# Kernel tuning notes

Hardware: AMD Instinct MI355X
Metric: run time of the kernel (lower is better)

The kernel has to match this reference:

```python
import jax, jax.numpy as jnp
import numpy as np

B, C, M, N = 8, 64, 256, 256
THRESHOLD = 0.8
EPS = 1e-5
PAD = 3  # kernel_size=7


def conv2d(x, w, b=None):
    # x: (B,Cin,H,W), w: (Cout,Cin,7,7), stride 1, 'same' padding 3
    y = jax.lax.conv_general_dilated(
        x, w, window_strides=(1, 1), padding=[(PAD, PAD), (PAD, PAD)],
        dimension_numbers=('NCHW', 'OIHW', 'NCHW'))
    if b is not None:
        y = y + b[None, :, None, None]
    return y


def region_norm(region, mask):
    # region: (B,C,M,N) zeroed outside region; mask: (B,C,M,N) binary
    s = jnp.sum(region, axis=(0, 2, 3))            # (C,)
    Sr = jnp.sum(mask, axis=(0, 2, 3))             # (C,)
    Sr = jnp.where(Sr == 0, 1.0, Sr)
    mu = (s / Sr)[None, :, None, None]
    t = region + (1.0 - mask) * mu                 # fill surroundings with region mean
    # BatchNorm2d(affine=False, track_running_stats=False): batch stats, biased var
    m = jnp.mean(t, axis=(0, 2, 3), keepdims=True)
    v = jnp.mean((t - m) ** 2, axis=(0, 2, 3), keepdims=True)
    bn = (t - m) * jax.lax.rsqrt(v + EPS)
    scale = jnp.sqrt(Sr / (region.shape[0] * region.shape[2] * region.shape[3]))
    return bn * scale[None, :, None, None]


def setup_inputs() -> dict:
    key = jax.random.key(0)
    k = jax.random.split(key, 6)
    x = jax.random.normal(k[0], (B, C, M, N), dtype=jnp.float32)
    # conv1: Conv2d(2,1,7,bias=False); gamma/beta: Conv2d(1,1,7) with bias
    w1 = jax.random.normal(k[1], (1, 2, 7, 7), dtype=jnp.float32) * 0.1
    wg = jax.random.normal(k[2], (1, 1, 7, 7), dtype=jnp.float32) * 0.1
    bg = jax.random.normal(k[3], (1,), dtype=jnp.float32) * 0.1
    wb = jax.random.normal(k[4], (1, 1, 7, 7), dtype=jnp.float32) * 0.1
    bb = jax.random.normal(k[5], (1,), dtype=jnp.float32) * 0.1
    return {"x": x, "w1": w1, "wg": wg, "bg": bg, "wb": wb, "bb": bb}


def reference(x, w1, wg, bg, wb, bb):
    # SelfAware_Affine
    avg_out = jnp.mean(x, axis=1, keepdims=True)       # (B,1,M,N)
    max_out = jnp.max(x, axis=1, keepdims=True)        # (B,1,M,N)
    sa_in = jnp.concatenate([avg_out, max_out], axis=1)
    sa_map = jax.nn.sigmoid(conv2d(sa_in, w1))         # (B,1,M,N)
    gamma = conv2d(sa_map, wg, bg)                     # (B,1,M,N)
    beta = conv2d(sa_map, wb, bb)                      # (B,1,M,N)
    # binary mask from detached importance map, expanded over channels
    mask = (jax.lax.stop_gradient(sa_map) >= THRESHOLD).astype(x.dtype)
    mask = jnp.broadcast_to(mask, x.shape)             # (B,C,M,N)
    rn_x = region_norm(x * mask, mask) + region_norm(x * (1.0 - mask), 1.0 - mask)
    return rn_x * (1.0 + gamma) + beta
```

## Files before the change

### kernel.cpp

```cpp
#include <hip/hip_runtime.h>
#include <cmath>

#define B_ 8
#define C_ 64
#define M_ 256
#define N_ 256
#define PLANE_ (M_*N_)
#define PIX_ (B_*PLANE_)
#define THRESH_ 0.8f
#define EPS_ 1e-5f

typedef float nt_f4 __attribute__((ext_vector_type(4)));

__global__ void k_avgmax(const float* __restrict__ x,
                         float* __restrict__ avgp, float* __restrict__ maxp,
                         float* __restrict__ acc) {
    if (blockIdx.x == 0) {
        if (threadIdx.x < 4 * C_) acc[threadIdx.x] = 0.f;
        if (threadIdx.x == 0) acc[4 * C_] = 0.f;
    }
    int idx4 = (blockIdx.x * blockDim.x + threadIdx.x) * 4;
    int b = idx4 >> 16;
    int p = idx4 & (PLANE_ - 1);
    const float* xb = x + (size_t)b * C_ * PLANE_ + p;
    float4 s = make_float4(0.f, 0.f, 0.f, 0.f);
    float4 mx = make_float4(-INFINITY, -INFINITY, -INFINITY, -INFINITY);
    #pragma unroll 16
    for (int c = 0; c < C_; ++c) {
        float4 v = *(const float4*)(xb + (size_t)c * PLANE_);
        s.x += v.x; s.y += v.y; s.z += v.z; s.w += v.w;
        mx.x = fmaxf(mx.x, v.x); mx.y = fmaxf(mx.y, v.y);
        mx.z = fmaxf(mx.z, v.z); mx.w = fmaxf(mx.w, v.w);
    }
    const float r = 1.f / C_;
    s.x *= r; s.y *= r; s.z *= r; s.w *= r;
    *(float4*)(avgp + idx4) = s;
    *(float4*)(maxp + idx4) = mx;
}

#define TW_ 64
#define TH_ 16
#define SAW_ (TW_+6)
#define SAH_ (TH_+6)
#define LDW_ (TW_+12)
#define LDH_ (TH_+12)

__global__ void k_sa_fused(const float* __restrict__ avgp, const float* __restrict__ maxp,
                           const float* __restrict__ w1,
                           const float* __restrict__ wg, const float* __restrict__ bgp,
                           const float* __restrict__ wb, const float* __restrict__ bbp,
                           float* __restrict__ gammap, float* __restrict__ betap,
                           unsigned char* __restrict__ maskp, int* __restrict__ cntp) {
    __shared__ float sA[LDH_][LDW_];
    __shared__ float sM[LDH_][LDW_];
    __shared__ float sSA[SAH_][SAW_];
    __shared__ float w[196];
    __shared__ int bcnt;
    int tid = threadIdx.x;
    if (tid < 98) w[tid] = w1[tid];
    else if (tid < 196) w[tid] = (tid < 147) ? wg[tid - 98] : wb[tid - 147];
    if (tid == 196) bcnt = 0;

    int tileid = blockIdx.x;
    int b = blockIdx.y;
    int ti0 = (tileid >> 2) * TH_;
    int tj0 = (tileid & 3) * TW_;
    const float* a = avgp + (size_t)b * PLANE_;
    const float* m = maxp + (size_t)b * PLANE_;

    for (int idx = tid; idx < LDH_ * LDW_; idx += 256) {
        int li = idx / LDW_;
        int lj = idx - li * LDW_;
        int gi = ti0 - 6 + li, gj = tj0 - 6 + lj;
        bool ok = ((unsigned)gi < (unsigned)M_) && ((unsigned)gj < (unsigned)N_);
        int o = gi * N_ + gj;
        sA[li][lj] = ok ? a[o] : 0.f;
        sM[li][lj] = ok ? m[o] : 0.f;
    }
    __syncthreads();

    for (int idx = tid; idx < SAH_ * SAW_; idx += 256) {
        int si = idx / SAW_;
        int sj = idx - si * SAW_;
        int gi = ti0 - 3 + si, gj = tj0 - 3 + sj;
        float v = 0.f;
        if ((unsigned)gi < (unsigned)M_ && (unsigned)gj < (unsigned)N_) {
            float acc = 0.f;
            #pragma unroll
            for (int dh = 0; dh < 7; ++dh) {
                #pragma unroll
                for (int dw = 0; dw < 7; ++dw) {
                    acc += sA[si + dh][sj + dw] * w[dh * 7 + dw]
                         + sM[si + dh][sj + dw] * w[49 + dh * 7 + dw];
                }
            }
            v = 1.f / (1.f + expf(-acc));
        }
        sSA[si][sj] = v;
    }
    __syncthreads();

    float bgv = bgp[0], bbv = bbp[0];
    int lcnt = 0;
    #pragma unroll
    for (int k = 0; k < 4; ++k) {
        int p = k * 256 + tid;
        int ti = p >> 6, tj = p & 63;
        float g = 0.f, be = 0.f;
        #pragma unroll
        for (int dh = 0; dh < 7; ++dh) {
            #pragma unroll
            for (int dw = 0; dw < 7; ++dw) {
                float v = sSA[ti + dh][tj + dw];
                g  += v * w[98 + dh * 7 + dw];
                be += v * w[147 + dh * 7 + dw];
            }
        }
        int idx = b * PLANE_ + (ti0 + ti) * N_ + (tj0 + tj);
        gammap[idx] = g + bgv;
        betap[idx]  = be + bbv;
        int mk = (sSA[ti + 3][tj + 3] >= THRESH_) ? 1 : 0;
        maskp[idx] = (unsigned char)mk;
        lcnt += mk;
    }
    for (int off = 32; off > 0; off >>= 1) lcnt += __shfl_down(lcnt, off, 64);
    if ((tid & 63) == 0) atomicAdd(&bcnt, lcnt);
    __syncthreads();
    if (tid == 0) atomicAdd(cntp, bcnt);
}

__global__ void k_sums(const float* __restrict__ x, const unsigned char* __restrict__ maskp,
                       float* __restrict__ S, float* __restrict__ Q,
                       float* __restrict__ S1, float* __restrict__ Q1) {
    int chunk = blockIdx.x;
    int c = blockIdx.y;
    int b = blockIdx.z;
    const float* xp = x + ((size_t)(b * C_ + c)) * PLANE_ + chunk * 8192;
    const unsigned char* mp = maskp + (size_t)b * PLANE_ + chunk * 8192;
    float s = 0.f, q = 0.f, s1 = 0.f, q1 = 0.f;
    #pragma unroll
    for (int k = 0; k < 8; ++k) {
        int t = (k * 256 + threadIdx.x) * 4;
        float4 v = *(const float4*)(xp + t);
        uchar4 mm = *(const uchar4*)(mp + t);
        float m0 = (float)mm.x, m1 = (float)mm.y, m2 = (float)mm.z, m3 = (float)mm.w;
        s  += v.x + v.y + v.z + v.w;
        q  += v.x * v.x + v.y * v.y + v.z * v.z + v.w * v.w;
        s1 += v.x * m0 + v.y * m1 + v.z * m2 + v.w * m3;
        q1 += v.x * v.x * m0 + v.y * v.y * m1 + v.z * v.z * m2 + v.w * v.w * m3;
    }
    for (int off = 32; off > 0; off >>= 1) {
        s  += __shfl_down(s, off, 64);
        q  += __shfl_down(q, off, 64);
        s1 += __shfl_down(s1, off, 64);
        q1 += __shfl_down(q1, off, 64);
    }
    __shared__ float ls[4][4];
    int wave = threadIdx.x >> 6, lane = threadIdx.x & 63;
    if (lane == 0) { ls[wave][0] = s; ls[wave][1] = q; ls[wave][2] = s1; ls[wave][3] = q1; }
    __syncthreads();
    if (threadIdx.x == 0) {
        float ts = 0.f, tq = 0.f, ts1 = 0.f, tq1 = 0.f;
        #pragma unroll
        for (int wv = 0; wv < 4; ++wv) { ts += ls[wv][0]; tq += ls[wv][1]; ts1 += ls[wv][2]; tq1 += ls[wv][3]; }
        atomicAdd(&S[c], ts); atomicAdd(&Q[c], tq);
        atomicAdd(&S1[c], ts1); atomicAdd(&Q1[c], tq1);
    }
}

__global__ void k_final(const float* __restrict__ x, const unsigned char* __restrict__ maskp,
                        const float* __restrict__ gammap, const float* __restrict__ betap,
                        const float* __restrict__ S, const float* __restrict__ Q,
                        const float* __restrict__ S1, const float* __restrict__ Q1,
                        const int* __restrict__ cntp,
                        float* __restrict__ out) {
    int c0 = blockIdx.y * 4;
    int b = blockIdx.z;
    const float P = (float)PIX_;
    int cnt1 = *cntp;
    float fc1 = (float)cnt1;
    float fc0 = P - fc1;
    float Sr1 = (cnt1 == 0) ? 1.f : fc1;
    float Sr0 = (cnt1 == PIX_) ? 1.f : fc0;
    float sq1 = sqrtf(Sr1 / P), sq0 = sqrtf(Sr0 / P);
    float ma[4], mb[4], ua[4], ub[4];
    #pragma unroll
    for (int cc = 0; cc < 4; ++cc) {
        int c = c0 + cc;
        float Sv = S[c], Qv = Q[c], S1v = S1[c], Q1v = Q1[c];
        float S0v = Sv - S1v, Q0v = Qv - Q1v;
        float mu1 = S1v / Sr1;
        float mu0 = S0v / Sr0;
        float m1 = (S1v + fc0 * mu1) / P;
        float v1 = fmaxf((Q1v + fc0 * mu1 * mu1) / P - m1 * m1, 0.f);
        float m0 = (S0v + fc1 * mu0) / P;
        float v0 = fmaxf((Q0v + fc1 * mu0 * mu0) / P - m0 * m0, 0.f);
        float A1 = rsqrtf(v1 + EPS_) * sq1;
        float A0 = rsqrtf(v0 + EPS_) * sq0;
        float B1 = (mu1 - m1) * A1;
        float B0 = (mu0 - m0) * A0;
        ma[cc] = A1; mb[cc] = -m1 * A1 + B0;
        ua[cc] = A0; ub[cc] = -m0 * A0 + B1;
    }

    int p0 = blockIdx.x * 1024 + threadIdx.x * 4;
    int pp = b * PLANE_ + p0;
    float4 gv = *(const float4*)(gammap + pp);
    float4 bv = *(const float4*)(betap + pp);
    uchar4 mv = *(const uchar4*)(maskp + pp);
    float4 G = make_float4(1.f + gv.x, 1.f + gv.y, 1.f + gv.z, 1.f + gv.w);
    #pragma unroll
    for (int cc = 0; cc < 4; ++cc) {
        size_t base = ((size_t)(b * C_ + c0 + cc)) * PLANE_ + p0;
        float4 xv = *(const float4*)(x + base);
        nt_f4 o;
        o.x = (mv.x ? xv.x * ma[cc] + mb[cc] : xv.x * ua[cc] + ub[cc]) * G.x + bv.x;
        o.y = (mv.y ? xv.y * ma[cc] + mb[cc] : xv.y * ua[cc] + ub[cc]) * G.y + bv.y;
        o.z = (mv.z ? xv.z * ma[cc] + mb[cc] : xv.z * ua[cc] + ub[cc]) * G.z + bv.z;
        o.w = (mv.w ? xv.w * ma[cc] + mb[cc] : xv.w * ua[cc] + ub[cc]) * G.w + bv.w;
        __builtin_nontemporal_store(o, (nt_f4*)(out + base));
    }
}

extern "C" void kernel_launch(void* const* d_in, const int* in_sizes, int n_in,
                              void* d_out, int out_size, void* d_ws, size_t ws_size,
                              hipStream_t stream) {
    const float* x  = (const float*)d_in[0];
    const float* w1 = (const float*)d_in[1];
    const float* wg = (const float*)d_in[2];
    const float* bg = (const float*)d_in[3];
    const float* wb = (const float*)d_in[4];
    const float* bb = (const float*)d_in[5];
    float* out = (float*)d_out;

    float* ws = (float*)d_ws;
    float* avgp   = ws;
    float* maxp   = avgp + PIX_;
    float* gammap = maxp + PIX_;
    float* betap  = gammap + PIX_;
    float* S   = betap + PIX_;
    float* Q   = S + C_;
    float* S1  = Q + C_;
    float* Q1  = S1 + C_;
    int*   cnt = (int*)(Q1 + C_);
    unsigned char* maskp = (unsigned char*)(cnt + 1);

    k_avgmax<<<PIX_ / (256 * 4), 256, 0, stream>>>(x, avgp, maxp, S);
    dim3 g2(64, B_);
    k_sa_fused<<<g2, 256, 0, stream>>>(avgp, maxp, w1, wg, bg, wb, bb,
                                       gammap, betap, maskp, cnt);
    dim3 g3(8, C_, B_);
    k_sums<<<g3, 256, 0, stream>>>(x, maskp, S, Q, S1, Q1);
    dim3 g5(PLANE_ / 1024, C_ / 4, B_);
    k_final<<<g5, 256, 0, stream>>>(x, maskp, gammap, betap, S, Q, S1, Q1, cnt, out);
}
```

Before: 328.3 us.

## Fuse channel statistics into avgmax and masked sums into SA kernel, drop k_sums

Removes the separate k_sums pass over x. The unmasked per-channel sum and sum of squares are now computed inside k_avgmax, which already streams all of x, using wave shuffles and per-block atomics. The masked sums are computed in k_sa_fused, only for tiles that contain mask pixels, by re-reading x for that tile. This saves one full read of x (about 134MB) for mostly-unmasked data, at the cost of per-channel shuffle reductions inside the avgmax loop, more atomics, and an added memset launch.

```diff
diff --git a/kernel.cpp b/kernel.cpp
--- a/kernel.cpp
+++ b/kernel.cpp
@@ -14,28 +14,42 @@
 
 __global__ void k_avgmax(const float* __restrict__ x,
                          float* __restrict__ avgp, float* __restrict__ maxp,
-                         float* __restrict__ acc) {
-    if (blockIdx.x == 0) {
-        if (threadIdx.x < 4 * C_) acc[threadIdx.x] = 0.f;
-        if (threadIdx.x == 0) acc[4 * C_] = 0.f;
-    }
-    int idx4 = (blockIdx.x * blockDim.x + threadIdx.x) * 4;
+                         float* __restrict__ S, float* __restrict__ Q) {
+    __shared__ float Sw[4][C_];
+    __shared__ float Qw[4][C_];
+    int tid = threadIdx.x;
+    int wave = tid >> 6, lane = tid & 63;
+    int idx4 = (blockIdx.x * blockDim.x + tid) * 4;
     int b = idx4 >> 16;
     int p = idx4 & (PLANE_ - 1);
     const float* xb = x + (size_t)b * C_ * PLANE_ + p;
     float4 s = make_float4(0.f, 0.f, 0.f, 0.f);
     float4 mx = make_float4(-INFINITY, -INFINITY, -INFINITY, -INFINITY);
-    #pragma unroll 16
+    #pragma unroll 8
     for (int c = 0; c < C_; ++c) {
         float4 v = *(const float4*)(xb + (size_t)c * PLANE_);
         s.x += v.x; s.y += v.y; s.z += v.z; s.w += v.w;
         mx.x = fmaxf(mx.x, v.x); mx.y = fmaxf(mx.y, v.y);
         mx.z = fmaxf(mx.z, v.z); mx.w = fmaxf(mx.w, v.w);
+        float sc = v.x + v.y + v.z + v.w;
+        float qc = v.x * v.x + v.y * v.y + v.z * v.z + v.w * v.w;
+        for (int off = 32; off > 0; off >>= 1) {
+            sc += __shfl_down(sc, off, 64);
+            qc += __shfl_down(qc, off, 64);
+        }
+        if (lane == 0) { Sw[wave][c] = sc; Qw[wave][c] = qc; }
     }
     const float r = 1.f / C_;
     s.x *= r; s.y *= r; s.z *= r; s.w *= r;
     *(float4*)(avgp + idx4) = s;
     *(float4*)(maxp + idx4) = mx;
+    __syncthreads();
+    if (tid < C_) {
+        atomicAdd(&S[tid], Sw[0][tid] + Sw[1][tid] + Sw[2][tid] + Sw[3][tid]);
+    } else if (tid < 2 * C_) {
+        int c = tid - C_;
+        atomicAdd(&Q[c], Qw[0][c] + Qw[1][c] + Qw[2][c] + Qw[3][c]);
+    }
 }
 
 #define TW_ 64
@@ -45,12 +59,14 @@
 #define LDW_ (TW_+12)
 #define LDH_ (TH_+12)
 
-__global__ void k_sa_fused(const float* __restrict__ avgp, const float* __restrict__ maxp,
+__global__ void k_sa_fused(const float* __restrict__ x,
+                           const float* __restrict__ avgp, const float* __restrict__ maxp,
                            const float* __restrict__ w1,
                            const float* __restrict__ wg, const float* __restrict__ bgp,
                            const float* __restrict__ wb, const float* __restrict__ bbp,
                            float* __restrict__ gammap, float* __restrict__ betap,
-                           unsigned char* __restrict__ maskp, int* __restrict__ cntp) {
+                           unsigned char* __restrict__ maskp, int* __restrict__ cntp,
+                           float* __restrict__ S1, float* __restrict__ Q1) {
     __shared__ float sA[LDH_][LDW_];
     __shared__ float sM[LDH_][LDW_];
     __shared__ float sSA[SAH_][SAW_];
@@ -126,45 +142,39 @@
     for (int off = 32; off > 0; off >>= 1) lcnt += __shfl_down(lcnt, off, 64);
     if ((tid & 63) == 0) atomicAdd(&bcnt, lcnt);
     __syncthreads();
+    if (bcnt == 0) return;
     if (tid == 0) atomicAdd(cntp, bcnt);
-}
-
-__global__ void k_sums(const float* __restrict__ x, const unsigned char* __restrict__ maskp,
-                       float* __restrict__ S, float* __restrict__ Q,
-                       float* __restrict__ S1, float* __restrict__ Q1) {
-    int chunk = blockIdx.x;
-    int c = blockIdx.y;
-    int b = blockIdx.z;
-    const float* xp = x + ((size_t)(b * C_ + c)) * PLANE_ + chunk * 8192;
-    const unsigned char* mp = maskp + (size_t)b * PLANE_ + chunk * 8192;
-    float s = 0.f, q = 0.f, s1 = 0.f, q1 = 0.f;
-    #pragma unroll
-    for (int k = 0; k < 8; ++k) {
-        int t = (k * 256 + threadIdx.x) * 4;
-        float4 v = *(const float4*)(xp + t);
-        uchar4 mm = *(const uchar4*)(mp + t);
-        float m0 = (float)mm.x, m1 = (float)mm.y, m2 = (float)mm.z, m3 = (float)mm.w;
-        s  += v.x + v.y + v.z + v.w;
-        q  += v.x * v.x + v.y * v.y + v.z * v.z + v.w * v.w;
-        s1 += v.x * m0 + v.y * m1 + v.z * m2 + v.w * m3;
-        q1 += v.x * v.x * m0 + v.y * v.y * m1 + v.z * v.z * m2 + v.w * v.w * m3;
-    }
-    for (int off = 32; off > 0; off >>= 1) {
-        s  += __shfl_down(s, off, 64);
-        q  += __shfl_down(q, off, 64);
-        s1 += __shfl_down(s1, off, 64);
-        q1 += __shfl_down(q1, off, 64);
-    }
-    __shared__ float ls[4][4];
-    int wave = threadIdx.x >> 6, lane = threadIdx.x & 63;
-    if (lane == 0) { ls[wave][0] = s; ls[wave][1] = q; ls[wave][2] = s1; ls[wave][3] = q1; }
-    __syncthreads();
-    if (threadIdx.x == 0) {
-        float ts = 0.f, tq = 0.f, ts1 = 0.f, tq1 = 0.f;
+
+    int wave = tid >> 6, lane = tid & 63;
+    int r0 = lane >> 4;
+    int c4 = (lane & 15) * 4;
+    float4 mm[4];
+    #pragma unroll
+    for (int i = 0; i < 4; ++i) {
+        int row = i * 4 + r0;
+        mm[i].x = (sSA[row + 3][c4 + 0 + 3] >= THRESH_) ? 1.f : 0.f;
+        mm[i].y = (sSA[row + 3][c4 + 1 + 3] >= THRESH_) ? 1.f : 0.f;
+        mm[i].z = (sSA[row + 3][c4 + 2 + 3] >= THRESH_) ? 1.f : 0.f;
+        mm[i].w = (sSA[row + 3][c4 + 3 + 3] >= THRESH_) ? 1.f : 0.f;
+    }
+    #pragma unroll
+    for (int k = 0; k < 16; ++k) {
+        int c = wave * 16 + k;
+        const float* xp = x + ((size_t)(b * C_ + c)) * PLANE_;
+        float s1 = 0.f, q1 = 0.f;
         #pragma unroll
-        for (int wv = 0; wv < 4; ++wv) { ts += ls[wv][0]; tq += ls[wv][1]; ts1 += ls[wv][2]; tq1 += ls[wv][3]; }
-        atomicAdd(&S[c], ts); atomicAdd(&Q[c], tq);
-        atomicAdd(&S1[c], ts1); atomicAdd(&Q1[c], tq1);
+        for (int i = 0; i < 4; ++i) {
+            int row = i * 4 + r0;
+            float4 v = *(const float4*)(xp + (ti0 + row) * N_ + tj0 + c4);
+            s1 += v.x * mm[i].x + v.y * mm[i].y + v.z * mm[i].z + v.w * mm[i].w;
+            q1 += v.x * v.x * mm[i].x + v.y * v.y * mm[i].y
+                + v.z * v.z * mm[i].z + v.w * v.w * mm[i].w;
+        }
+        for (int off = 32; off > 0; off >>= 1) {
+            s1 += __shfl_down(s1, off, 64);
+            q1 += __shfl_down(q1, off, 64);
+        }
+        if (lane == 0) { atomicAdd(&S1[c], s1); atomicAdd(&Q1[c], q1); }
     }
 }
 
@@ -245,12 +255,12 @@
     int*   cnt = (int*)(Q1 + C_);
     unsigned char* maskp = (unsigned char*)(cnt + 1);
 
-    k_avgmax<<<PIX_ / (256 * 4), 256, 0, stream>>>(x, avgp, maxp, S);
+    hipMemsetAsync(S, 0, (4 * C_ + 1) * sizeof(float), stream);
+
+    k_avgmax<<<PIX_ / (256 * 4), 256, 0, stream>>>(x, avgp, maxp, S, Q);
     dim3 g2(64, B_);
-    k_sa_fused<<<g2, 256, 0, stream>>>(avgp, maxp, w1, wg, bg, wb, bb,
-                                       gammap, betap, maskp, cnt);
-    dim3 g3(8, C_, B_);
-    k_sums<<<g3, 256, 0, stream>>>(x, maskp, S, Q, S1, Q1);
+    k_sa_fused<<<g2, 256, 0, stream>>>(x, avgp, maxp, w1, wg, bg, wb, bb,
+                                       gammap, betap, maskp, cnt, S1, Q1);
     dim3 g5(PLANE_ / 1024, C_ / 4, B_);
     k_final<<<g5, 256, 0, stream>>>(x, maskp, gammap, betap, S, Q, S1, Q1, cnt, out);
 }
```

After: 515.3 us. 1.57x slower.
